# Performance work log

Measured on AMD Instinct MI355X. Metric: run time of the kernel, lower is better.

Reference implementation:

```python
import jax, jax.numpy as jnp
import numpy as np

# init_kwargs constants
MIN_T = 0.01
MAX_T = 0.5
TGT_MIN = 0.005
TGT_MAX = 0.03
W_MIN = 15.0
W_MAX = 5.0
W_CONT = 5.0
W_SIZE = 7.0
LESION_T = 0.3


def setup_inputs() -> dict:
    key = jax.random.key(0)
    pred = jax.random.uniform(key, (16, 1, 128, 128, 128), dtype=jnp.float32)
    return {"pred": pred}


def reference(pred):
    # pred: [B, 1, D, H, W]
    s = pred[:, 0]  # [B, D, H, W]
    B = s.shape[0]
    axes = (1, 2, 3)

    # -- min/max activation penalties (per-sample threshold means) --
    act = jnp.mean((s > MIN_T).astype(s.dtype), axis=axes)          # [B]
    loss = jax.nn.relu(TGT_MIN - act) * W_MIN
    high = jnp.mean((s > MAX_T).astype(s.dtype), axis=axes)
    loss = loss + jax.nn.relu(high - TGT_MAX) * W_MAX

    # -- continuity penalty: mean abs finite differences along D,H,W --
    d_grad = jnp.mean(jnp.abs(s[:, 1:] - s[:, :-1]), axis=axes)
    h_grad = jnp.mean(jnp.abs(s[:, :, 1:] - s[:, :, :-1]), axis=axes)
    w_grad = jnp.mean(jnp.abs(s[:, :, :, 1:] - s[:, :, :, :-1]), axis=axes)
    avg_grad = (d_grad + h_grad + w_grad) / 3.0
    has_lesion = jnp.any(s > LESION_T, axis=axes)
    loss = loss + jnp.where(has_lesion, jnp.minimum(avg_grad, 1.0), 0.0) * W_CONT

    # -- size-variance penalty over masked active values (unbiased std, torch.std) --
    mask = (s > MIN_T).astype(s.dtype)
    cnt = jnp.sum(mask, axis=axes)                                   # [B]
    cnt_safe = jnp.maximum(cnt, 1.0)
    m = jnp.sum(s * mask, axis=axes) / cnt_safe                      # masked mean [B]
    sq = jnp.sum(mask * (s - m[:, None, None, None]) ** 2, axis=axes)
    gate = (act > 0.001) & (cnt > 1.0)
    var = jnp.where(gate, sq / jnp.maximum(cnt - 1.0, 1.0), 1.0)     # guard sqrt/grad when gated off
    std = jnp.sqrt(var)
    rel_std = std / (m + 1e-6)
    pen = jnp.exp(-5.0 * rel_std)
    loss = loss + jnp.where(gate, pen, 0.0) * W_SIZE

    return jnp.sum(loss) / B
```

## Files before the change

### kernel.cpp

```cpp
#include <hip/hip_runtime.h>
#include <math.h>

#define MIN_T    0.01f
#define MAX_T    0.5f
#define LESION_T 0.3f

constexpr int NB       = 16;
constexpr int DIM      = 128;
constexpr int PLANE_F4 = DIM * DIM / 4;
constexpr int VOX      = DIM * DIM * DIM;
constexpr int THREADS  = 256;
constexpr int HWBLKS   = PLANE_F4 / THREADS;
constexpr int DSEGS    = 8;
constexpr int DPS      = DIM / DSEGS;
constexpr int NACC     = 8;

struct Acc {
    float cnt_min = 0.f, cnt_max = 0.f, sum_d = 0.f, sum_h = 0.f,
          sum_w = 0.f, sm = 0.f, sm2 = 0.f, les = 0.f;
};

__device__ __forceinline__ void stats(const float4 v, const float4 vh,
                                      bool do_h, bool do_w, Acc& a)
{
    const float xs[4] = { v.x, v.y, v.z, v.w };
    #pragma unroll
    for (int j = 0; j < 4; ++j) {
        const float x    = xs[j];
        const bool  gmin = (x > MIN_T);
        const float xm   = gmin ? x : 0.0f;
        a.cnt_min += gmin ? 1.0f : 0.0f;
        a.sm      += xm;
        a.sm2      = fmaf(xm, x, a.sm2);
        a.cnt_max += (x > MAX_T)    ? 1.0f : 0.0f;
        a.les     += (x > LESION_T) ? 1.0f : 0.0f;
    }
    a.sum_w += fabsf(v.y - v.x) + fabsf(v.z - v.y) + fabsf(v.w - v.z);
    const float nx = __shfl_down(v.x, 1, 64);
    if (do_w) a.sum_w += fabsf(nx - v.w);
    if (do_h) a.sum_h += fabsf(vh.x - v.x) + fabsf(vh.y - v.y)
                       + fabsf(vh.z - v.z) + fabsf(vh.w - v.w);
}

template<int NPAIR, bool LAST>
__device__ __forceinline__ void seg_body(const float4* __restrict__ s4,
                                         size_t base, int hoff,
                                         bool do_h, bool do_w, Acc& a)
{
    float4 v0 = s4[base];
    float4 h0 = s4[base + hoff];
    #pragma unroll
    for (int k = 0; k < NPAIR; ++k) {
        const size_t nb = base + (size_t)(k + 1) * PLANE_F4;
        const float4 v1 = s4[nb];
        const float4 h1 = s4[nb + hoff];
        stats(v0, h0, do_h, do_w, a);
        a.sum_d += fabsf(v1.x - v0.x) + fabsf(v1.y - v0.y)
                 + fabsf(v1.z - v0.z) + fabsf(v1.w - v0.w);
        v0 = v1; h0 = h1;
    }
    if (LAST) stats(v0, h0, do_h, do_w, a);
}

__global__ __launch_bounds__(THREADS)
void partial_kernel(const float* __restrict__ pred, double* __restrict__ acc)
{
    const int seg   = blockIdx.x;
    const int hwblk = blockIdx.y;
    const int b     = blockIdx.z;
    const int tid   = (int)threadIdx.x;

    const float4* __restrict__ s4 =
        reinterpret_cast<const float4*>(pred + (size_t)b * VOX);

    const int  h    = hwblk * 8 + (tid >> 5);
    const bool do_h = (h < DIM - 1);
    const bool do_w = ((tid & 31) != 31);
    const int  hoff = do_h ? 32 : 0;

    const size_t base = (size_t)(seg * DPS) * PLANE_F4
                      + (size_t)hwblk * THREADS + tid;

    Acc a;
    if (seg != DSEGS - 1)
        seg_body<DPS, false>(s4, base, hoff, do_h, do_w, a);
    else
        seg_body<DPS - 1, true>(s4, base, hoff, do_h, do_w, a);

    float vals[NACC] = { a.cnt_min, a.cnt_max, a.sum_d, a.sum_h,
                         a.sum_w, a.sm, a.sm2, a.les };
    #pragma unroll
    for (int vi = 0; vi < NACC; ++vi) {
        float x = vals[vi];
        #pragma unroll
        for (int offs = 32; offs > 0; offs >>= 1)
            x += __shfl_down(x, offs, 64);
        vals[vi] = x;
    }

    __shared__ float smem[4][NACC];
    const int wave = tid >> 6;
    const int lane = tid & 63;
    if (lane == 0) {
        #pragma unroll
        for (int vi = 0; vi < NACC; ++vi) smem[wave][vi] = vals[vi];
    }
    __syncthreads();
    if (tid < NACC) {
        const float t = smem[0][tid] + smem[1][tid] +
                        smem[2][tid] + smem[3][tid];
        atomicAdd(&acc[(size_t)b * NACC + tid], (double)t);
    }
}

__global__ __launch_bounds__(64)
void finalize_kernel(const double* __restrict__ acc, float* __restrict__ out)
{
    float l = 0.0f;
    if (threadIdx.x < NB) {
        const double* a = acc + (size_t)threadIdx.x * NACC;
        const double cnt    = a[0];
        const double cntmax = a[1];
        const double sd     = a[2];
        const double sh     = a[3];
        const double sw     = a[4];
        const double sm     = a[5];
        const double sm2    = a[6];
        const double les    = a[7];

        const double inv_vox = 1.0 / (double)VOX;
        const double act  = cnt    * inv_vox;
        const double high = cntmax * inv_vox;

        double loss = fmax(0.005 - act, 0.0) * 15.0
                    + fmax(high - 0.03, 0.0) * 5.0;

        const double grad_den = 127.0 * 128.0 * 128.0;
        const double avg_grad = (sd + sh + sw) / (3.0 * grad_den);
        if (les > 0.5)
            loss += fmin(avg_grad, 1.0) * 5.0;

        const double cnt_safe = fmax(cnt, 1.0);
        const double m  = sm / cnt_safe;
        double sq = sm2 - 2.0 * m * sm + m * m * cnt;
        if (sq < 0.0) sq = 0.0;

        const bool gate = (act > 0.001) && (cnt > 1.0);
        if (gate) {
            const double var     = sq / fmax(cnt - 1.0, 1.0);
            const double rel_std = sqrt(var) / (m + 1e-6);
            loss += exp(-5.0 * rel_std) * 7.0;
        }
        l = (float)loss;
    }
    #pragma unroll
    for (int offs = 32; offs > 0; offs >>= 1)
        l += __shfl_down(l, offs, 64);
    if (threadIdx.x == 0)
        out[0] = l / (float)NB;
}

extern "C" void kernel_launch(void* const* d_in, const int* in_sizes, int n_in,
                              void* d_out, int out_size, void* d_ws, size_t ws_size,
                              hipStream_t stream)
{
    const float* pred = (const float*)d_in[0];
    float* out        = (float*)d_out;
    double* acc       = (double*)d_ws;

    hipMemsetAsync(d_ws, 0, (size_t)NB * NACC * sizeof(double), stream);

    dim3 grid(DSEGS, HWBLKS, NB);
    partial_kernel<<<grid, THREADS, 0, stream>>>(pred, acc);
    finalize_kernel<<<1, 64, 0, stream>>>(acc, out);
}
```

Measured before the change: 197.7 us.

## Replace double atomics and memset with per-block partial slots and finalize reduction

Each block now writes its eight float partial sums to a dedicated workspace slot, replacing the double-precision atomicAdd into per-sample accumulators. This removes the hipMemsetAsync launch. The finalize kernel now reads all slots with 256 threads and reduces them in double. The number of depth segments also doubles, giving more, shorter blocks for better occupancy and latency hiding. In exchange, finalize does more work, partials are rounded to float before summing, and the slot bit-packing only holds for these fixed sizes.

```diff
diff --git a/kernel.cpp b/kernel.cpp
--- a/kernel.cpp
+++ b/kernel.cpp
@@ -11,9 +11,10 @@
 constexpr int VOX      = DIM * DIM * DIM;
 constexpr int THREADS  = 256;
 constexpr int HWBLKS   = PLANE_F4 / THREADS;
-constexpr int DSEGS    = 8;
+constexpr int DSEGS    = 16;
 constexpr int DPS      = DIM / DSEGS;
 constexpr int NACC     = 8;
+constexpr int NSLOTS   = NB * DSEGS * HWBLKS;
 
 struct Acc {
     float cnt_min = 0.f, cnt_max = 0.f, sum_d = 0.f, sum_h = 0.f,
@@ -63,7 +64,7 @@
 }
 
 __global__ __launch_bounds__(THREADS)
-void partial_kernel(const float* __restrict__ pred, double* __restrict__ acc)
+void partial_kernel(const float* __restrict__ pred, float* __restrict__ pacc)
 {
     const int seg   = blockIdx.x;
     const int hwblk = blockIdx.y;
@@ -107,26 +108,49 @@
     }
     __syncthreads();
     if (tid < NACC) {
-        const float t = smem[0][tid] + smem[1][tid] +
-                        smem[2][tid] + smem[3][tid];
-        atomicAdd(&acc[(size_t)b * NACC + tid], (double)t);
-    }
-}
-
-__global__ __launch_bounds__(64)
-void finalize_kernel(const double* __restrict__ acc, float* __restrict__ out)
-{
-    float l = 0.0f;
-    if (threadIdx.x < NB) {
-        const double* a = acc + (size_t)threadIdx.x * NACC;
-        const double cnt    = a[0];
-        const double cntmax = a[1];
-        const double sd     = a[2];
-        const double sh     = a[3];
-        const double sw     = a[4];
-        const double sm     = a[5];
-        const double sm2    = a[6];
-        const double les    = a[7];
+        const int slot = (b << 8) | (seg << 4) | hwblk;
+        pacc[(size_t)slot * NACC + tid] =
+            smem[0][tid] + smem[1][tid] + smem[2][tid] + smem[3][tid];
+    }
+}
+
+__global__ __launch_bounds__(THREADS)
+void finalize_kernel(const float* __restrict__ pacc, float* __restrict__ out)
+{
+    const int tid = (int)threadIdx.x;
+    const int b   = tid >> 4;
+    const int j   = tid & 15;
+
+    double s[NACC];
+    #pragma unroll
+    for (int i = 0; i < NACC; ++i) s[i] = 0.0;
+
+    const float4* p4 = reinterpret_cast<const float4*>(pacc);
+    #pragma unroll
+    for (int k = 0; k < DSEGS; ++k) {
+        const int slot = (b << 8) | (k << 4) | j;
+        const float4 lo = p4[slot * 2];
+        const float4 hi = p4[slot * 2 + 1];
+        s[0] += lo.x; s[1] += lo.y; s[2] += lo.z; s[3] += lo.w;
+        s[4] += hi.x; s[5] += hi.y; s[6] += hi.z; s[7] += hi.w;
+    }
+    #pragma unroll
+    for (int i = 0; i < NACC; ++i) {
+        #pragma unroll
+        for (int offs = 8; offs > 0; offs >>= 1)
+            s[i] += __shfl_down(s[i], offs, 16);
+    }
+
+    __shared__ float lss[NB];
+    if (j == 0) {
+        const double cnt    = s[0];
+        const double cntmax = s[1];
+        const double sd     = s[2];
+        const double sh     = s[3];
+        const double sw     = s[4];
+        const double sm     = s[5];
+        const double sm2    = s[6];
+        const double les    = s[7];
 
         const double inv_vox = 1.0 / (double)VOX;
         const double act  = cnt    * inv_vox;
@@ -151,13 +175,15 @@
             const double rel_std = sqrt(var) / (m + 1e-6);
             loss += exp(-5.0 * rel_std) * 7.0;
         }
-        l = (float)loss;
-    }
-    #pragma unroll
-    for (int offs = 32; offs > 0; offs >>= 1)
-        l += __shfl_down(l, offs, 64);
-    if (threadIdx.x == 0)
-        out[0] = l / (float)NB;
+        lss[b] = (float)loss;
+    }
+    __syncthreads();
+    if (tid == 0) {
+        float t = 0.f;
+        #pragma unroll
+        for (int i = 0; i < NB; ++i) t += lss[i];
+        out[0] = t / (float)NB;
+    }
 }
 
 extern "C" void kernel_launch(void* const* d_in, const int* in_sizes, int n_in,
@@ -166,11 +192,9 @@
 {
     const float* pred = (const float*)d_in[0];
     float* out        = (float*)d_out;
-    double* acc       = (double*)d_ws;
-
-    hipMemsetAsync(d_ws, 0, (size_t)NB * NACC * sizeof(double), stream);
+    float* pacc       = (float*)d_ws;
 
     dim3 grid(DSEGS, HWBLKS, NB);
-    partial_kernel<<<grid, THREADS, 0, stream>>>(pred, acc);
-    finalize_kernel<<<1, 64, 0, stream>>>(acc, out);
-}
+    partial_kernel<<<grid, THREADS, 0, stream>>>(pred, pacc);
+    finalize_kernel<<<1, THREADS, 0, stream>>>(pacc, out);
+}
```

Result: no change. 197.1 us (-0.3%).
